# Optimization experiments

Measured on AMD Instinct MI355X. Metric: run time of the kernel, lower is better.

Reference implementation:

```python
import jax, jax.numpy as jnp
import numpy as np

SOFTEN = 10000.0
COLOR_NORM = 1.0
COLOR_JITTER = 0.0
EPS = 1e-8


def setup_inputs() -> dict:
    key = jax.random.key(0)
    k1, k2, k3, k4, k5 = jax.random.split(key, 5)
    B, C, H, W = 4, 64, 512, 512
    K, HID = 16, 128
    img = jax.random.uniform(k1, (B, 3, H, W), dtype=jnp.float32)
    feat = jax.random.normal(k2, (B, C, H, W), dtype=jnp.float32)
    W1 = jax.random.normal(k3, (HID, C), dtype=jnp.float32) * 0.05
    b1 = jax.random.normal(k4, (HID,), dtype=jnp.float32) * 0.05
    W2 = jax.random.normal(k5, (K, HID), dtype=jnp.float32) * 0.05
    return {"img": img, "feat": feat, "W1": W1, "b1": b1, "W2": W2, "training": 0}


def reference(img, feat, W1, b1, W2, training):
    # color_mask head: two 1x1 convs (pure channel contractions)
    h = jax.nn.relu(jnp.einsum('bchw,oc->bohw', feat, W1) + b1[None, :, None, None])
    logits = jnp.einsum('bohw,ko->bkhw', h, W2)           # [B,K,H,W]
    m = jax.nn.softmax(SOFTEN * logits, axis=1)           # Softmax2d over channel dim
    K = m.shape[1]
    M = jnp.argmax(m, axis=1)                             # [B,H,W]
    # one-hot indicator, channel-first: [B,K,H,W]
    indicator = (jnp.arange(K)[None, :, None, None] == M[:, None]).astype(m.dtype)
    if training:
        w = m
        norm = COLOR_NORM
    else:
        w = indicator
        norm = 1.0
    # weighted spatial reduction instead of materializing [B,K,3,H,W]
    num = jnp.einsum('bkhw,bchw->bkc', w, img)            # [B,K,3]
    den = jnp.sum(w, axis=(2, 3))                         # [B,K]
    palette = num / (den[:, :, None] + EPS) / norm        # [B,K,3]
    if training:
        palette_used = palette + COLOR_JITTER * np.random.randn()
    else:
        palette_used = palette
    transformed_img = jnp.einsum('bkhw,bkc->bchw', w, palette_used)  # [B,3,H,W]
    color_palette = palette[:, :, :, None, None]          # keepdim [B,K,3,1,1]
    return transformed_img, m, color_palette
```

## Files before the change

kernel.cpp:

```cpp
#include <hip/hip_runtime.h>

#define HW_  262144
#define C_   64
#define HID_ 128
#define K_   16
#define B_   4
#define NPIX (B_*HW_)

typedef __attribute__((ext_vector_type(8)))  short bf16x8;
typedef __attribute__((ext_vector_type(16))) float f32x16;

#define W1F_BYTE 2048
#define W2F_BYTE 34816
#define LBL_BYTE 51200
#define WS_NEED_FAST ((size_t)LBL_BYTE + (size_t)NPIX*4)

__device__ __forceinline__ unsigned short f2bf(float x) {
    unsigned u = __float_as_uint(x);
    unsigned r = u + 0x7FFFu + ((u >> 16) & 1u);
    return (unsigned short)(r >> 16);
}
__device__ __forceinline__ float bf2f(unsigned short h) {
    return __uint_as_float(((unsigned)h) << 16);
}
__device__ __forceinline__ f32x16 mfma32(bf16x8 a, bf16x8 b, f32x16 c) {
    return __builtin_amdgcn_mfma_f32_32x32x16_bf16(a, b, c, 0, 0, 0);
}


__global__ __launch_bounds__(256) void prep_fast(
    const float* __restrict__ W1, const float* __restrict__ W2,
    float* __restrict__ wsf)
{
    int gi = blockIdx.x*256 + threadIdx.x;
    if (gi < 256) wsf[gi] = 0.0f;
    unsigned short* w1f = (unsigned short*)((char*)wsf + W1F_BYTE);
    unsigned short* w2f = (unsigned short*)((char*)wsf + W2F_BYTE);
    if (gi < 8192) {
        int j = gi & 7, l = (gi >> 3) & 63, s = (gi >> 9) & 3, m = (gi >> 11) & 3;
        int o = 32*m + (l & 31);
        int c = 16*s + 8*(l >> 5) + j;
        float w  = W1[o*C_ + c];
        unsigned short hi = f2bf(w);
        unsigned short lo = f2bf(w - bf2f(hi));
        int base = ((m*4 + s)*2)*512 + l*8 + j;
        w1f[base]       = hi;
        w1f[base + 512] = lo;
    } else if (gi < 12288) {
        int i = gi - 8192;
        int j = i & 7, l = (i >> 3) & 63, t = (i >> 9) & 7;
        int k = l & 31;
        int o = 16*t + 8*(l >> 5) + j;
        float w = (k < K_) ? W2[k*HID_ + o] : 0.0f;
        unsigned short hi = f2bf(w);
        unsigned short lo = f2bf(w - bf2f(hi));
        int base = (t*2)*512 + l*8 + j;
        w2f[base]       = hi;
        w2f[base + 512] = lo;
    }
}

__global__ __launch_bounds__(256, 3) void mlp_mfma(
    const float* __restrict__ feat, const float* __restrict__ img,
    const float* __restrict__ b1,
    const unsigned short* __restrict__ w1f, const unsigned short* __restrict__ w2f,
    float* __restrict__ m_out, float* __restrict__ accum, int* __restrict__ labels)
{
    __shared__ float b1s[HID_];
    __shared__ float bins[K_*4];

    int t = threadIdx.x, lane = t & 63, w = t >> 6;
    int col = lane & 31, half = lane >> 5;
    if (t < HID_) b1s[t] = b1[t];
    if (t < K_*4) bins[t] = 0.0f;
    __syncthreads();

    int blk = blockIdx.x;
    int b   = blk >> 11;
    int px  = (blk & 2047)*128 + w*32 + col;
    const float* fb = feat + ((size_t)b*C_ << 18) + px;

    float fv[32];
#pragma unroll
    for (int s = 0; s < 4; ++s)
#pragma unroll
        for (int j = 0; j < 8; ++j)
            fv[s*8 + j] = fb[(size_t)(16*s + 8*half + j) << 18];

    bf16x8 bh[4], bl[4];
#pragma unroll
    for (int s = 0; s < 4; ++s)
#pragma unroll
        for (int j = 0; j < 8; ++j) {
            float x = fv[s*8 + j];
            unsigned short hi = f2bf(x);
            bh[s][j] = (short)hi;
            bl[s][j] = (short)f2bf(x - bf2f(hi));
        }

    f32x16 acc[4];
#pragma unroll
    for (int m = 0; m < 4; ++m) acc[m] = 0.0f;

    const bf16x8* w1v = (const bf16x8*)w1f;
#pragma unroll
    for (int s = 0; s < 4; ++s)
#pragma unroll
        for (int m = 0; m < 4; ++m) {
            const bf16x8* p = w1v + ((m*4 + s)*2)*64 + lane;
            bf16x8 ah = p[0];
            bf16x8 al = p[64];
            acc[m] = mfma32(ah, bh[s], acc[m]);
            acc[m] = mfma32(al, bh[s], acc[m]);
            acc[m] = mfma32(ah, bl[s], acc[m]);
        }

    f32x16 acc2 = 0.0f;
    const bf16x8* w2v = (const bf16x8*)w2f;
#pragma unroll
    for (int tg = 0; tg < 8; ++tg) {
        int m = tg >> 1, sub = tg & 1;
        unsigned pk[8];
#pragma unroll
        for (int i = 0; i < 8; ++i) {
            int r = 8*sub + i;
            int o = 32*m + (i & 3) + 16*sub + 8*(i >> 2) + 4*half;
            float hv = fmaxf(acc[m][r] + b1s[o], 0.0f);
            unsigned short hi = f2bf(hv);
            unsigned short lo = f2bf(hv - bf2f(hi));
            pk[i] = ((unsigned)hi) | (((unsigned)lo) << 16);
        }
        bf16x8 bh2, bl2;
#pragma unroll
        for (int j = 0; j < 4; ++j) {
            unsigned ov = half ? pk[j+4] : pk[j];
            unsigned sv = half ? pk[j]   : pk[j+4];
            unsigned rv = (unsigned)__shfl_xor((int)sv, 32);
            unsigned lowsrc  = half ? rv : ov;
            unsigned highsrc = half ? ov : rv;
            bh2[j]   = (short)(lowsrc  & 0xffffu);
            bl2[j]   = (short)(lowsrc  >> 16);
            bh2[j+4] = (short)(highsrc & 0xffffu);
            bl2[j+4] = (short)(highsrc >> 16);
        }
        const bf16x8* p = w2v + (tg*2)*64 + lane;
        bf16x8 ah = p[0];
        bf16x8 al = p[64];
        acc2 = mfma32(ah, bh2, acc2);
        acc2 = mfma32(al, bh2, acc2);
        acc2 = mfma32(ah, bl2, acc2);
    }

    float lg[8]; int kk[8];
#pragma unroll
    for (int r = 0; r < 8; ++r) {
        lg[r] = acc2[r];
        kk[r] = (r & 3) + 8*(r >> 2) + 4*half;
    }
    float mx = lg[0]; int ki = kk[0];
#pragma unroll
    for (int r = 1; r < 8; ++r)
        if (lg[r] > mx) { mx = lg[r]; ki = kk[r]; }
    float mxo = __shfl_xor(mx, 32);
    int   kio = __shfl_xor(ki, 32);
    if (mxo > mx || (mxo == mx && kio < ki)) { mx = mxo; ki = kio; }

    float es[8], ss = 0.0f;
#pragma unroll
    for (int r = 0; r < 8; ++r) {
        es[r] = __expf(1.0e4f * (lg[r] - mx));
        ss += es[r];
    }
    ss += __shfl_xor(ss, 32);
    float inv = 1.0f / ss;

    size_t mbase = (size_t)(b*K_) << 18;
#pragma unroll
    for (int r = 0; r < 8; ++r)
        m_out[mbase + ((size_t)kk[r] << 18) + px] = es[r] * inv;

    if (half == 0) {
        labels[((size_t)b << 18) + px] = ki;
        const float* ip = img + ((size_t)(b*3) << 18) + px;
        atomicAdd(&bins[ki*4+0], ip[0]);
        atomicAdd(&bins[ki*4+1], ip[(size_t)1 << 18]);
        atomicAdd(&bins[ki*4+2], ip[(size_t)2 << 18]);
        atomicAdd(&bins[ki*4+3], 1.0f);
    }
    __syncthreads();
    if (t < K_*4) atomicAdd(&accum[b*K_*4 + t], bins[t]);
}

__global__ __launch_bounds__(64) void palette_kernel(
    const float* __restrict__ accum, float* __restrict__ pal_out,
    float* __restrict__ palf)
{
    int t = threadIdx.x;
    float den  = accum[t*4+3];
    float invd = 1.0f / (den + 1e-8f);
#pragma unroll
    for (int c = 0; c < 3; ++c) {
        float pal = accum[t*4+c] * invd;
        palf[t*3+c]    = pal;
        pal_out[t*3+c] = pal;
    }
}

__global__ __launch_bounds__(256) void recolor_lbl_kernel(
    const int* __restrict__ labels, const float* __restrict__ palf,
    float* __restrict__ timg)
{
    int g = blockIdx.x*256 + threadIdx.x;
    int b = g >> 18;
    int p = g & (HW_-1);
    int ks = labels[g];
#pragma unroll
    for (int c = 0; c < 3; ++c)
        timg[((size_t)(b*3+c) << 18) + p] = palf[(b*K_ + ks)*3 + c];
}

__global__ __launch_bounds__(256) void prep_scalar(
    const float* __restrict__ W1, const float* __restrict__ b1,
    const float* __restrict__ W2, float* __restrict__ wsf)
{
    int t = threadIdx.x;
    wsf[t] = 0.0f;
    for (int i = t; i < HID_*C_; i += 256) wsf[256 + i] = W1[i];
    if (t < HID_) wsf[8448 + t] = b1[t];
    for (int i = t; i < K_*HID_; i += 256) {
        int k = i / HID_, o = i % HID_;
        wsf[8576 + o*K_ + k] = W2[i];
    }
}

__global__ __launch_bounds__(256) void mlp_scalar(
    const float* __restrict__ feat, const float* __restrict__ img,
    const float* __restrict__ wsf, float* __restrict__ m_out,
    float* __restrict__ accum)
{
    __shared__ float bins[K_*4];
    int t = threadIdx.x;
    if (t < K_*4) bins[t] = 0.0f;
    __syncthreads();
    int g = blockIdx.x*256 + t;
    int b = g >> 18, p = g & (HW_-1);
    const float* fp = feat + ((size_t)(b*C_) << 18) + p;
    float f[C_];
#pragma unroll
    for (int c = 0; c < C_; ++c) f[c] = fp[(size_t)c << 18];
    const float* W1f = wsf + 256;
    const float* b1f = wsf + 8448;
    const float* W2T = wsf + 8576;
    float logits[K_];
#pragma unroll
    for (int k = 0; k < K_; ++k) logits[k] = 0.0f;
    for (int o = 0; o < HID_; ++o) {
        float h = b1f[o];
#pragma unroll
        for (int c = 0; c < C_; ++c) h = fmaf(f[c], W1f[o*C_ + c], h);
        h = fmaxf(h, 0.0f);
#pragma unroll
        for (int k = 0; k < K_; ++k) logits[k] = fmaf(h, W2T[o*K_ + k], logits[k]);
    }
    float lmax = logits[0]; int kstar = 0;
#pragma unroll
    for (int k = 1; k < K_; ++k)
        if (logits[k] > lmax) { lmax = logits[k]; kstar = k; }
    float ex[K_], esum = 0.0f;
#pragma unroll
    for (int k = 0; k < K_; ++k) { ex[k] = __expf(1.0e4f*(logits[k]-lmax)); esum += ex[k]; }
    float inv = 1.0f / esum;
#pragma unroll
    for (int k = 0; k < K_; ++k)
        m_out[((size_t)(b*K_ + k) << 18) + p] = ex[k] * inv;
    const float* ip = img + ((size_t)(b*3) << 18) + p;
    atomicAdd(&bins[kstar*4+0], ip[0]);
    atomicAdd(&bins[kstar*4+1], ip[(size_t)1 << 18]);
    atomicAdd(&bins[kstar*4+2], ip[(size_t)2 << 18]);
    atomicAdd(&bins[kstar*4+3], 1.0f);
    __syncthreads();
    if (t < K_*4) atomicAdd(&accum[b*K_*4 + t], bins[t]);
}

__global__ __launch_bounds__(256) void recolor_m_kernel(
    const float* __restrict__ m_in, const float* __restrict__ palf,
    float* __restrict__ timg)
{
    int g = blockIdx.x*256 + threadIdx.x;
    int b = g >> 18, p = g & (HW_-1);
    const float* mp = m_in + ((size_t)(b*K_) << 18) + p;
    float best = -1.0f; int ks = 0;
#pragma unroll
    for (int k = 0; k < K_; ++k) {
        float v = mp[(size_t)k << 18];
        if (v > best) { best = v; ks = k; }
    }
#pragma unroll
    for (int c = 0; c < 3; ++c)
        timg[((size_t)(b*3+c) << 18) + p] = palf[(b*K_ + ks)*3 + c];
}

extern "C" void kernel_launch(void* const* d_in, const int* in_sizes, int n_in,
                              void* d_out, int out_size, void* d_ws, size_t ws_size,
                              hipStream_t stream)
{
    const float* img  = (const float*)d_in[0];
    const float* feat = (const float*)d_in[1];
    const float* W1   = (const float*)d_in[2];
    const float* b1   = (const float*)d_in[3];
    const float* W2   = (const float*)d_in[4];

    float* out0 = (float*)d_out;
    float* out1 = out0 + (size_t)B_*3*HW_;
    float* out2 = out1 + (size_t)B_*K_*HW_;
    float* wsf  = (float*)d_ws;

    if (ws_size >= WS_NEED_FAST) {
        const unsigned short* w1f = (const unsigned short*)((char*)d_ws + W1F_BYTE);
        const unsigned short* w2f = (const unsigned short*)((char*)d_ws + W2F_BYTE);
        int* lbl = (int*)((char*)d_ws + LBL_BYTE);
        float* palf = wsf + 256;
        prep_fast<<<48, 256, 0, stream>>>(W1, W2, wsf);
        mlp_mfma<<<NPIX/128, 256, 0, stream>>>(feat, img, b1,
                                               w1f, w2f, out1, wsf, lbl);
        palette_kernel<<<1, 64, 0, stream>>>(wsf, out2, palf);
        recolor_lbl_kernel<<<NPIX/256, 256, 0, stream>>>(lbl, palf, out0);
    } else {
        prep_scalar<<<1, 256, 0, stream>>>(W1, b1, W2, wsf);
        mlp_scalar<<<NPIX/256, 256, 0, stream>>>(feat, img, wsf, out1, wsf);
        palette_kernel<<<1, 64, 0, stream>>>(wsf, out2, wsf + 10624);
        recolor_m_kernel<<<NPIX/256, 256, 0, stream>>>(out1, wsf + 10624, out0);
    }
}
```

Baseline: 518.8 us.

## Interleave MLP layers to cut register pressure and slice palette atomics

Restructures the MFMA MLP so each layer-1 accumulator block is immediately consumed by the layer-2 MFMAs, keeping only one f32x16 live instead of four. This allows the launch bound to rise from 3 to 5 blocks per CU for better latency hiding. Palette accumulation atomics are spread over 8 workspace slices to reduce contention, and the palette kernel sums the slices. The higher occupancy target risks register spills.

```diff
diff --git a/kernel.cpp b/kernel.cpp
--- a/kernel.cpp
+++ b/kernel.cpp
@@ -6,13 +6,15 @@
 #define K_   16
 #define B_   4
 #define NPIX (B_*HW_)
+#define NSLICE 8
 
 typedef __attribute__((ext_vector_type(8)))  short bf16x8;
 typedef __attribute__((ext_vector_type(16))) float f32x16;
 
-#define W1F_BYTE 2048
-#define W2F_BYTE 34816
-#define LBL_BYTE 51200
+#define PALF_FLT 2048
+#define W1F_BYTE 10240
+#define W2F_BYTE 43008
+#define LBL_BYTE 59392
 #define WS_NEED_FAST ((size_t)LBL_BYTE + (size_t)NPIX*4)
 
 __device__ __forceinline__ unsigned short f2bf(float x) {
@@ -33,7 +35,7 @@
     float* __restrict__ wsf)
 {
     int gi = blockIdx.x*256 + threadIdx.x;
-    if (gi < 256) wsf[gi] = 0.0f;
+    if (gi < NSLICE*256) wsf[gi] = 0.0f;
     unsigned short* w1f = (unsigned short*)((char*)wsf + W1F_BYTE);
     unsigned short* w2f = (unsigned short*)((char*)wsf + W2F_BYTE);
     if (gi < 8192) {
@@ -60,7 +62,7 @@
     }
 }
 
-__global__ __launch_bounds__(256, 3) void mlp_mfma(
+__global__ __launch_bounds__(256, 5) void mlp_mfma(
     const float* __restrict__ feat, const float* __restrict__ img,
     const float* __restrict__ b1,
     const unsigned short* __restrict__ w1f, const unsigned short* __restrict__ w2f,
@@ -98,57 +100,55 @@
             bl[s][j] = (short)f2bf(x - bf2f(hi));
         }
 
-    f32x16 acc[4];
-#pragma unroll
-    for (int m = 0; m < 4; ++m) acc[m] = 0.0f;
-
     const bf16x8* w1v = (const bf16x8*)w1f;
-#pragma unroll
-    for (int s = 0; s < 4; ++s)
-#pragma unroll
-        for (int m = 0; m < 4; ++m) {
+    const bf16x8* w2v = (const bf16x8*)w2f;
+    f32x16 acc2 = 0.0f;
+
+#pragma unroll
+    for (int m = 0; m < 4; ++m) {
+        f32x16 accm = 0.0f;
+#pragma unroll
+        for (int s = 0; s < 4; ++s) {
             const bf16x8* p = w1v + ((m*4 + s)*2)*64 + lane;
             bf16x8 ah = p[0];
             bf16x8 al = p[64];
-            acc[m] = mfma32(ah, bh[s], acc[m]);
-            acc[m] = mfma32(al, bh[s], acc[m]);
-            acc[m] = mfma32(ah, bl[s], acc[m]);
+            accm = mfma32(ah, bh[s], accm);
+            accm = mfma32(al, bh[s], accm);
+            accm = mfma32(ah, bl[s], accm);
         }
-
-    f32x16 acc2 = 0.0f;
-    const bf16x8* w2v = (const bf16x8*)w2f;
-#pragma unroll
-    for (int tg = 0; tg < 8; ++tg) {
-        int m = tg >> 1, sub = tg & 1;
-        unsigned pk[8];
-#pragma unroll
-        for (int i = 0; i < 8; ++i) {
-            int r = 8*sub + i;
-            int o = 32*m + (i & 3) + 16*sub + 8*(i >> 2) + 4*half;
-            float hv = fmaxf(acc[m][r] + b1s[o], 0.0f);
-            unsigned short hi = f2bf(hv);
-            unsigned short lo = f2bf(hv - bf2f(hi));
-            pk[i] = ((unsigned)hi) | (((unsigned)lo) << 16);
+#pragma unroll
+        for (int sub = 0; sub < 2; ++sub) {
+            int tg = 2*m + sub;
+            unsigned pk[8];
+#pragma unroll
+            for (int i = 0; i < 8; ++i) {
+                int r = 8*sub + i;
+                int o = 32*m + (i & 3) + 16*sub + 8*(i >> 2) + 4*half;
+                float hv = fmaxf(accm[r] + b1s[o], 0.0f);
+                unsigned short hi = f2bf(hv);
+                unsigned short lo = f2bf(hv - bf2f(hi));
+                pk[i] = ((unsigned)hi) | (((unsigned)lo) << 16);
+            }
+            bf16x8 bh2, bl2;
+#pragma unroll
+            for (int j = 0; j < 4; ++j) {
+                unsigned ov = half ? pk[j+4] : pk[j];
+                unsigned sv = half ? pk[j]   : pk[j+4];
+                unsigned rv = (unsigned)__shfl_xor((int)sv, 32);
+                unsigned lowsrc  = half ? rv : ov;
+                unsigned highsrc = half ? ov : rv;
+                bh2[j]   = (short)(lowsrc  & 0xffffu);
+                bl2[j]   = (short)(lowsrc  >> 16);
+                bh2[j+4] = (short)(highsrc & 0xffffu);
+                bl2[j+4] = (short)(highsrc >> 16);
+            }
+            const bf16x8* p2 = w2v + (tg*2)*64 + lane;
+            bf16x8 ah2 = p2[0];
+            bf16x8 al2 = p2[64];
+            acc2 = mfma32(ah2, bh2, acc2);
+            acc2 = mfma32(al2, bh2, acc2);
+            acc2 = mfma32(ah2, bl2, acc2);
         }
-        bf16x8 bh2, bl2;
-#pragma unroll
-        for (int j = 0; j < 4; ++j) {
-            unsigned ov = half ? pk[j+4] : pk[j];
-            unsigned sv = half ? pk[j]   : pk[j+4];
-            unsigned rv = (unsigned)__shfl_xor((int)sv, 32);
-            unsigned lowsrc  = half ? rv : ov;
-            unsigned highsrc = half ? ov : rv;
-            bh2[j]   = (short)(lowsrc  & 0xffffu);
-            bl2[j]   = (short)(lowsrc  >> 16);
-            bh2[j+4] = (short)(highsrc & 0xffffu);
-            bl2[j+4] = (short)(highsrc >> 16);
-        }
-        const bf16x8* p = w2v + (tg*2)*64 + lane;
-        bf16x8 ah = p[0];
-        bf16x8 al = p[64];
-        acc2 = mfma32(ah, bh2, acc2);
-        acc2 = mfma32(al, bh2, acc2);
-        acc2 = mfma32(ah, bl2, acc2);
     }
 
     float lg[8]; int kk[8];
@@ -188,22 +188,24 @@
         atomicAdd(&bins[ki*4+3], 1.0f);
     }
     __syncthreads();
-    if (t < K_*4) atomicAdd(&accum[b*K_*4 + t], bins[t]);
+    if (t < K_*4) atomicAdd(&accum[(blk & (NSLICE-1))*256 + b*K_*4 + t], bins[t]);
 }
 
 __global__ __launch_bounds__(64) void palette_kernel(
-    const float* __restrict__ accum, float* __restrict__ pal_out,
-    float* __restrict__ palf)
+    const float* __restrict__ accum, int nslices,
+    float* __restrict__ pal_out, float* __restrict__ palf)
 {
     int t = threadIdx.x;
-    float den  = accum[t*4+3];
-    float invd = 1.0f / (den + 1e-8f);
-#pragma unroll
-    for (int c = 0; c < 3; ++c) {
-        float pal = accum[t*4+c] * invd;
-        palf[t*3+c]    = pal;
-        pal_out[t*3+c] = pal;
-    }
+    float s0 = 0.0f, s1 = 0.0f, s2 = 0.0f, s3 = 0.0f;
+    for (int sl = 0; sl < nslices; ++sl) {
+        const float* a = accum + sl*256 + t*4;
+        s0 += a[0]; s1 += a[1]; s2 += a[2]; s3 += a[3];
+    }
+    float invd = 1.0f / (s3 + 1e-8f);
+    float p0 = s0*invd, p1 = s1*invd, p2 = s2*invd;
+    palf[t*3+0] = p0; pal_out[t*3+0] = p0;
+    palf[t*3+1] = p1; pal_out[t*3+1] = p1;
+    palf[t*3+2] = p2; pal_out[t*3+2] = p2;
 }
 
 __global__ __launch_bounds__(256) void recolor_lbl_kernel(
@@ -319,16 +321,16 @@
         const unsigned short* w1f = (const unsigned short*)((char*)d_ws + W1F_BYTE);
         const unsigned short* w2f = (const unsigned short*)((char*)d_ws + W2F_BYTE);
         int* lbl = (int*)((char*)d_ws + LBL_BYTE);
-        float* palf = wsf + 256;
+        float* palf = wsf + PALF_FLT;
         prep_fast<<<48, 256, 0, stream>>>(W1, W2, wsf);
         mlp_mfma<<<NPIX/128, 256, 0, stream>>>(feat, img, b1,
                                                w1f, w2f, out1, wsf, lbl);
-        palette_kernel<<<1, 64, 0, stream>>>(wsf, out2, palf);
+        palette_kernel<<<1, 64, 0, stream>>>(wsf, NSLICE, out2, palf);
         recolor_lbl_kernel<<<NPIX/256, 256, 0, stream>>>(lbl, palf, out0);
     } else {
         prep_scalar<<<1, 256, 0, stream>>>(W1, b1, W2, wsf);
         mlp_scalar<<<NPIX/256, 256, 0, stream>>>(feat, img, wsf, out1, wsf);
-        palette_kernel<<<1, 64, 0, stream>>>(wsf, out2, wsf + 10624);
+        palette_kernel<<<1, 64, 0, stream>>>(wsf, 1, out2, wsf + 10624);
         recolor_m_kernel<<<NPIX/256, 256, 0, stream>>>(out1, wsf + 10624, out0);
     }
 }
```

After: 452.8 us. -12.7%, faster.
